# Kernel optimization log

Hardware: AMD Instinct MI355X
Metric: run time of the kernel (lower is better)

Reference implementation:

```python
import jax, jax.numpy as jnp
import numpy as np

NEG_SLOPE = 0.2  # PyG GATConv default leaky_relu slope


def gat_conv(h_in, src, dst, W, a_src, a_dst, b, N):
    # h_in: [N, Fin]; src/dst: [E] (self-loops already appended)
    h = h_in @ W                      # [N, Fout]
    alpha_src = h @ a_src             # [N]
    alpha_dst = h @ a_dst             # [N]
    e = jax.nn.leaky_relu(alpha_src[src] + alpha_dst[dst], NEG_SLOPE)  # [E]
    # segment softmax over incoming edges of each destination node
    m = jax.ops.segment_max(e, dst, num_segments=N)
    m = jnp.where(jnp.isfinite(m), m, 0.0)
    p = jnp.exp(e - m[dst])
    denom = jax.ops.segment_sum(p, dst, num_segments=N)
    alpha = p / jnp.maximum(denom[dst], 1e-16)
    out = jax.ops.segment_sum(alpha[:, None] * h[src], dst, num_segments=N)
    return out + b


def setup_inputs() -> dict:
    key = jax.random.key(0)
    ks = jax.random.split(key, 16)
    N, E, V, D, H, C, G = 100000, 1600000, 128, 50, 16, 10, 512
    x = jax.random.normal(ks[0], (N, V), dtype=jnp.float32)
    edge_index = jax.random.randint(ks[1], (2, E), 0, N, dtype=jnp.int32)
    batch = jnp.sort(jax.random.randint(ks[2], (N,), 0, G, dtype=jnp.int32))
    s = lambda fan: 1.0 / np.sqrt(fan)
    return {
        "x": x, "edge_index": edge_index, "batch": batch,
        "embedding": jax.random.normal(ks[3], (V, D), dtype=jnp.float32),
        "W1": jax.random.normal(ks[4], (D, H), dtype=jnp.float32) * s(D),
        "a_src1": jax.random.normal(ks[5], (H,), dtype=jnp.float32) * s(H),
        "a_dst1": jax.random.normal(ks[6], (H,), dtype=jnp.float32) * s(H),
        "b1": jnp.zeros((H,), dtype=jnp.float32),
        "W2": jax.random.normal(ks[7], (H, H), dtype=jnp.float32) * s(H),
        "a_src2": jax.random.normal(ks[8], (H,), dtype=jnp.float32) * s(H),
        "a_dst2": jax.random.normal(ks[9], (H,), dtype=jnp.float32) * s(H),
        "b2": jnp.zeros((H,), dtype=jnp.float32),
        "W3": jax.random.normal(ks[10], (H, C), dtype=jnp.float32) * s(H),
        "a_src3": jax.random.normal(ks[11], (C,), dtype=jnp.float32) * s(C),
        "a_dst3": jax.random.normal(ks[12], (C,), dtype=jnp.float32) * s(C),
        "b3": jnp.zeros((C,), dtype=jnp.float32),
    }


def reference(x, edge_index, batch, embedding, W1, a_src1, a_dst1, b1,
              W2, a_src2, a_dst2, b2, W3, a_src3, a_dst3, b3):
    N = x.shape[0]
    G = 512  # num graphs
    # embedding lookup via argmax over one-hot-ish features
    idx = jnp.argmax(x, axis=1)
    h = embedding[idx]                               # [N, 50]
    # add self-loops once (PyG GATConv default)
    loops = jnp.arange(N, dtype=edge_index.dtype)
    src = jnp.concatenate([edge_index[0], loops])
    dst = jnp.concatenate([edge_index[1], loops])
    h = jax.nn.relu(gat_conv(h, src, dst, W1, a_src1, a_dst1, b1, N))
    # dropout: eval mode -> identity
    h = jax.nn.relu(gat_conv(h, src, dst, W2, a_src2, a_dst2, b2, N))
    h = gat_conv(h, src, dst, W3, a_src3, a_dst3, b3, N)  # [N, C]
    # global mean pool over graphs
    sums = jax.ops.segment_sum(h, batch, num_segments=G)
    cnts = jax.ops.segment_sum(jnp.ones((N,), h.dtype), batch, num_segments=G)
    pooled = sums / jnp.maximum(cnts, 1.0)[:, None]
    return jax.nn.softmax(pooled, axis=1)
```

## Files before the change

kernel.cpp:

```cpp
#include <hip/hip_runtime.h>
#include <math.h>

#define NEG_SLOPE 0.2f
#define NBUK_MAX 512

typedef float v4f __attribute__((ext_vector_type(4)));
typedef _Float16 h4v __attribute__((ext_vector_type(4)));

#define RECB 64

template <int B2>
__global__ void __launch_bounds__(1024)
k_histarg(const float* __restrict__ x, const int* __restrict__ edst, int E,
          int* __restrict__ histT, int NBUK, int* __restrict__ idx, int N, int V) {
    __shared__ int sh[NBUK_MAX];
    int t = threadIdx.x;
    if ((int)blockIdx.x < B2) {
        int b = blockIdx.x;
        for (int k = t; k < NBUK; k += 1024) sh[k] = 0;
        __syncthreads();
        long long ebeg = (long long)b * E / B2, eend = (long long)(b + 1) * E / B2;
        for (long long i = ebeg + t; i < eend; i += 1024)
            atomicAdd(&sh[edst[i] >> 8], 1);
        __syncthreads();
        for (int k = t; k < NBUK; k += 1024) histT[(long long)k * B2 + b] = sh[k];
    } else {
        int node = ((int)blockIdx.x - B2) * 32 + (t >> 5);
        int lane = t & 31;
        if (node >= N) return;
        const v4f* row = (const v4f*)(x + (long long)node * V);
        float bv = -INFINITY;
        int bi = 0x7fffffff;
        int nq = V >> 2;
        for (int q = lane; q < nq; q += 32) {
            v4f v = row[q];
            int base = q << 2;
            if (v.x > bv || (v.x == bv && base     < bi)) { bv = v.x; bi = base;     }
            if (v.y > bv || (v.y == bv && base + 1 < bi)) { bv = v.y; bi = base + 1; }
            if (v.z > bv || (v.z == bv && base + 2 < bi)) { bv = v.z; bi = base + 2; }
            if (v.w > bv || (v.w == bv && base + 3 < bi)) { bv = v.w; bi = base + 3; }
        }
        for (int off = 16; off > 0; off >>= 1) {
            float ov = __shfl_down(bv, off, 32);
            int   oi = __shfl_down(bi, off, 32);
            if (ov > bv || (ov == bv && oi < bi)) { bv = ov; bi = oi; }
        }
        if (lane == 0) idx[node] = bi;
    }
}

template <int FIN, int FOUT>
__global__ void __launch_bounds__(256)
k_scan_tr(const int* __restrict__ vals, int* __restrict__ excl, int* __restrict__ bsums, int M,
          const float* __restrict__ emb, const int* __restrict__ idx,
          const float* __restrict__ W, const float* __restrict__ a_src,
          const float* __restrict__ a_dst, char* __restrict__ rec,
          int N, int NB_SCAN) {
    __shared__ int s[256];
    __shared__ float sW[FIN * FOUT];
    __shared__ float sa[FOUT], sd[FOUT];
    int t = threadIdx.x;
    if ((int)blockIdx.x < NB_SCAN) {
        int i = blockIdx.x * 256 + t;
        int v = (i < M) ? vals[i] : 0;
        s[t] = v;
        __syncthreads();
        for (int off = 1; off < 256; off <<= 1) {
            int a = (t >= off) ? s[t - off] : 0;
            __syncthreads();
            s[t] += a;
            __syncthreads();
        }
        if (i < M) excl[i] = s[t] - v;
        if (t == 255) bsums[blockIdx.x] = s[255];
    } else {
        for (int i = t; i < FIN * FOUT; i += 256) sW[i] = W[i];
        if (t < FOUT) { sa[t] = a_src[t]; sd[t] = a_dst[t]; }
        __syncthreads();
        int n = ((int)blockIdx.x - NB_SCAN) * 256 + t;
        if (n >= N) return;
        float acc[FOUT];
#pragma unroll
        for (int f = 0; f < FOUT; f++) acc[f] = 0.f;
        const float* hr = emb + (long long)idx[n] * FIN;
        for (int k = 0; k < FIN; k++) {
            float v = hr[k];
#pragma unroll
            for (int f = 0; f < FOUT; f++) acc[f] += v * sW[k * FOUT + f];
        }
        float s1 = 0.f, s2 = 0.f;
        _Float16 hh[16];
#pragma unroll
        for (int f = 0; f < 16; f++) hh[f] = (_Float16)0.f;
#pragma unroll
        for (int f = 0; f < FOUT; f++) {
            hh[f] = (_Float16)acc[f];
            s1 += acc[f] * sa[f];
            s2 += acc[f] * sd[f];
        }
        char* r = rec + (long long)n * RECB;
        *(uint4*)(r)      = ((uint4*)hh)[0];
        *(uint4*)(r + 16) = ((uint4*)hh)[1];
        float2 am; am.x = s1; am.y = s2;
        *(float2*)(r + 32) = am;
    }
}

template <int B2>
__global__ void __launch_bounds__(1024)
k_scatB(const int* __restrict__ esrc, const int* __restrict__ edst, int E,
        const int* __restrict__ sexcl, const int* __restrict__ bsums,
        int* __restrict__ tmp, int NBUK) {
    __shared__ int cur[NBUK_MAX];
    __shared__ int bex[512];
    int t = threadIdx.x, b = blockIdx.x;
    if (t < 512) bex[t] = (t < NBUK) ? bsums[t] : 0;
    __syncthreads();
    for (int off = 1; off < 512; off <<= 1) {
        int a = (t < 512 && t >= off) ? bex[t - off] : 0;
        __syncthreads();
        if (t < 512) bex[t] += a;
        __syncthreads();
    }
    for (int k = t; k < NBUK; k += 1024)
        cur[k] = sexcl[(long long)k * B2 + b] + (k ? bex[k - 1] : 0);
    __syncthreads();
    long long ebeg = (long long)b * E / B2, eend = (long long)(b + 1) * E / B2;
    for (long long i = ebeg + t; i < eend; i += 1024) {
        int d = edst[i];
        int pos = atomicAdd(&cur[d >> 8], 1);
        tmp[pos] = ((d & 255) << 17) | esrc[i];
    }
}

template <int B2>
__global__ void __launch_bounds__(256)
k_binB(const int* __restrict__ sexcl, const int* __restrict__ bsums,
       const int* __restrict__ tmp, int* __restrict__ perm, char* __restrict__ recA,
       int* __restrict__ csr_src, int N, int NBUK, int E) {
    __shared__ int bx[512];
    __shared__ int cnt[256];
    __shared__ int h1[256];
    __shared__ int h2[256];
    __shared__ int sdv[256];
    __shared__ int ssc[256];
    __shared__ int cur[256];
    int t = threadIdx.x, b = blockIdx.x;
    bx[t]       = (t < NBUK)       ? bsums[t]       : 0;
    bx[t + 256] = (t + 256 < NBUK) ? bsums[t + 256] : 0;
    __syncthreads();
    for (int off = 1; off < 512; off <<= 1) {
        int a0 = (t >= off) ? bx[t - off] : 0;
        int a1 = (t + 256 >= off) ? bx[t + 256 - off] : 0;
        __syncthreads();
        bx[t] += a0;
        bx[t + 256] += a1;
        __syncthreads();
    }
    int t0 = sexcl[(long long)b * B2] + (b ? bx[b - 1] : 0);
    int t1 = (b + 1 < NBUK) ? (sexcl[(long long)(b + 1) * B2] + bx[b]) : E;
    cnt[t] = 0;
    __syncthreads();
    for (int i = t0 + t; i < t1; i += 256) atomicAdd(&cnt[tmp[i] >> 17], 1);
    __syncthreads();
    int d = b * 256 + t;
    bool valid = d < N;
    int dg = cnt[t];

    h1[t] = 0;
    __syncthreads();
    int key = 255 - min(dg, 255);
    if (valid) atomicAdd(&h1[key], 1);
    __syncthreads();
    int v = h1[t];
    h2[t] = v;
    __syncthreads();
    for (int off = 1; off < 256; off <<= 1) {
        int a = (t >= off) ? h2[t - off] : 0;
        __syncthreads();
        h2[t] += a;
        __syncthreads();
    }
    h1[t] = h2[t] - v;
    __syncthreads();
    int r = 0;
    if (valid) r = atomicAdd(&h1[key], 1);

    sdv[t] = 0;
    __syncthreads();
    if (valid) sdv[r] = dg;
    __syncthreads();
    int sv = sdv[t];
    ssc[t] = sv;
    __syncthreads();
    for (int off = 1; off < 256; off <<= 1) {
        int a = (t >= off) ? ssc[t - off] : 0;
        __syncthreads();
        ssc[t] += a;
        __syncthreads();
    }
    if (valid) {
        int base = t0 + ssc[r] - dg;
        cur[t] = base;
        perm[b * 256 + r] = d;
        int2 m; m.x = base; m.y = base + dg;
        *(int2*)(recA + (long long)d * RECB + 40) = m;
    }
    __syncthreads();
    for (int i = t0 + t; i < t1; i += 256) {
        int p = tmp[i];
        int pos = atomicAdd(&cur[p >> 17], 1);
        csr_src[pos] = p & 0x1FFFF;
    }
}

template <typename EPI>
__device__ __forceinline__ void gat_core4(const char* __restrict__ rec,
                                          const int* __restrict__ csr_src,
                                          int d, int l4, EPI epilogue) {
    const char* rd = rec + (long long)d * RECB;
    int4 meta = *(const int4*)(rd + 32);
    float as_d = __int_as_float(meta.x);
    float ad   = __int_as_float(meta.y);
    int r0 = meta.z, r1 = meta.w;

    float e0 = as_d + ad;
    e0 = (e0 >= 0.f) ? e0 : NEG_SLOPE * e0;
    float p0 = __expf(e0);
    h4v hd = *(const h4v*)(rd + l4 * 8);
    float a0 = p0 * (float)hd[0], a1 = p0 * (float)hd[1];
    float a2 = p0 * (float)hd[2], a3 = p0 * (float)hd[3];
    float psum = (l4 == 0) ? p0 : 0.f;

    int rem = r1 - r0;
    if (rem > 0) {
        int j = r0;
        int s = (l4 < rem) ? csr_src[j + l4] : d;
        float av = *(const float*)(rec + (long long)s * RECB + 32);
        while (true) {
            int remn = rem - 4;
            int s2 = d; float av2 = 0.f;
            if (remn > 0) {
                s2 = (l4 < remn) ? csr_src[j + 4 + l4] : d;
                av2 = *(const float*)(rec + (long long)s2 * RECB + 32);
            }
            float e = av + ad;
            e = (e >= 0.f) ? e : NEG_SLOPE * e;
            float p = (l4 < rem) ? __expf(e) : 0.f;
            psum += p;
#pragma unroll
            for (int k = 0; k < 4; k++) {
                float pk = __shfl(p, k, 4);
                int   sk = __shfl(s, k, 4);
                h4v hh = *(const h4v*)(rec + (long long)sk * RECB + l4 * 8);
                a0 += pk * (float)hh[0];
                a1 += pk * (float)hh[1];
                a2 += pk * (float)hh[2];
                a3 += pk * (float)hh[3];
            }
            if (remn <= 0) break;
            j += 4; rem = remn; s = s2; av = av2;
        }
    }
    psum += __shfl_xor(psum, 1, 4);
    psum += __shfl_xor(psum, 2, 4);
    float inv = 1.f / fmaxf(psum, 1e-16f);
    epilogue(d, r0, r1, a0 * inv, a1 * inv, a2 * inv, a3 * inv);
}

template <int FN>
__global__ void __launch_bounds__(256)
k_gat_ft(const char* __restrict__ rec, const int* __restrict__ csr_src,
         const int* __restrict__ perm, const float* __restrict__ bias,
         const float* __restrict__ Wn, const float* __restrict__ an_src,
         const float* __restrict__ an_dst, char* __restrict__ rec_next, int N) {
    __shared__ float sW[16 * 16];
    __shared__ float sa[16], sd[16], sb[16];
    int t = threadIdx.x;
    {
        int k = t >> 4, f = t & 15;
        sW[t] = (f < FN) ? Wn[k * FN + f] : 0.f;
    }
    if (t < 16) {
        sa[t] = (t < FN) ? an_src[t] : 0.f;
        sd[t] = (t < FN) ? an_dst[t] : 0.f;
        sb[t] = bias[t];
    }
    __syncthreads();

    int gid = blockIdx.x * 256 + t;
    int grp = gid >> 2, l4 = gid & 3;
    if (grp >= N) return;
    int d = perm[grp];

    gat_core4(rec, csr_src, d, l4,
        [&](int dd, int r0, int r1, float v0, float v1, float v2, float v3) {
            int f0 = l4 * 4;
            float vv[4];
            vv[0] = fmaxf(v0 + sb[f0    ], 0.f);
            vv[1] = fmaxf(v1 + sb[f0 + 1], 0.f);
            vv[2] = fmaxf(v2 + sb[f0 + 2], 0.f);
            vv[3] = fmaxf(v3 + sb[f0 + 3], 0.f);
            float o0 = 0.f, o1 = 0.f, o2 = 0.f, o3 = 0.f;
#pragma unroll
            for (int q = 0; q < 4; q++) {
#pragma unroll
                for (int i = 0; i < 4; i++) {
                    float vk = __shfl(vv[i], q, 4);
                    const float* wr = &sW[(q * 4 + i) * 16 + f0];
                    o0 += vk * wr[0];
                    o1 += vk * wr[1];
                    o2 += vk * wr[2];
                    o3 += vk * wr[3];
                }
            }
            float c1 = o0 * sa[f0] + o1 * sa[f0 + 1] + o2 * sa[f0 + 2] + o3 * sa[f0 + 3];
            float c2 = o0 * sd[f0] + o1 * sd[f0 + 1] + o2 * sd[f0 + 2] + o3 * sd[f0 + 3];
            c1 += __shfl_xor(c1, 1, 4); c1 += __shfl_xor(c1, 2, 4);
            c2 += __shfl_xor(c2, 1, 4); c2 += __shfl_xor(c2, 2, 4);
            char* rn = rec_next + (long long)dd * RECB;
            h4v ho = { (_Float16)o0, (_Float16)o1, (_Float16)o2, (_Float16)o3 };
            *(h4v*)(rn + l4 * 8) = ho;
            if (l4 == 0) {
                int4 m;
                m.x = __float_as_int(c1); m.y = __float_as_int(c2);
                m.z = r0; m.w = r1;
                *(int4*)(rn + 32) = m;
            }
        });
}

__global__ void __launch_bounds__(256)
k_gat_last(const char* __restrict__ rec, const int* __restrict__ csr_src,
           const int* __restrict__ perm, float* __restrict__ out, int N) {
    int gid = blockIdx.x * 256 + threadIdx.x;
    int grp = gid >> 2, l4 = gid & 3;
    if (grp >= N) return;
    int d = perm[grp];
    gat_core4(rec, csr_src, d, l4,
        [&](int dd, int r0, int r1, float v0, float v1, float v2, float v3) {
            v4f o = { v0, v1, v2, v3 };
            ((v4f*)out)[(long long)dd * 4 + l4] = o;
        });
}

__global__ void k_pool(const float* __restrict__ h3, const int* __restrict__ batch,
                       const float* __restrict__ b3, float* __restrict__ out, int N, int C) {
    int g = blockIdx.x;
    int lo = 0, hi = N;
    while (lo < hi) { int mid = (lo + hi) >> 1; if (batch[mid] < g) lo = mid + 1; else hi = mid; }
    int start = lo;
    hi = N;
    while (lo < hi) { int mid = (lo + hi) >> 1; if (batch[mid] < g + 1) lo = mid + 1; else hi = mid; }
    int end = lo;

    float sum[16];
    for (int f = 0; f < C; f++) sum[f] = 0.f;
    for (int n = start + threadIdx.x; n < end; n += blockDim.x) {
        const float* r = h3 + (long long)n * 16;
        for (int f = 0; f < C; f++) sum[f] += r[f];
    }
    __shared__ float red[256 * 16];
    for (int f = 0; f < C; f++) red[threadIdx.x * 16 + f] = sum[f];
    __syncthreads();
    for (int str = blockDim.x / 2; str > 0; str >>= 1) {
        if ((int)threadIdx.x < str)
            for (int f = 0; f < C; f++) red[threadIdx.x * 16 + f] += red[(threadIdx.x + str) * 16 + f];
        __syncthreads();
    }
    if (threadIdx.x == 0) {
        float cnt = fmaxf((float)(end - start), 1.f);
        float vals[16];
        float mx = -INFINITY;
        for (int f = 0; f < C; f++) { vals[f] = red[f] / cnt + b3[f]; mx = fmaxf(mx, vals[f]); }
        float se = 0.f;
        for (int f = 0; f < C; f++) { vals[f] = __expf(vals[f] - mx); se += vals[f]; }
        for (int f = 0; f < C; f++) out[(long long)g * C + f] = vals[f] / se;
    }
}

extern "C" void kernel_launch(void* const* d_in, const int* in_sizes, int n_in,
                              void* d_out, int out_size, void* d_ws, size_t ws_size,
                              hipStream_t stream) {
    const float* x    = (const float*)d_in[0];
    const int*   eidx = (const int*)d_in[1];
    const int*   batch= (const int*)d_in[2];
    const float* emb  = (const float*)d_in[3];
    const float* W1   = (const float*)d_in[4];
    const float* as1  = (const float*)d_in[5];
    const float* ad1  = (const float*)d_in[6];
    const float* b1   = (const float*)d_in[7];
    const float* W2   = (const float*)d_in[8];
    const float* as2  = (const float*)d_in[9];
    const float* ad2  = (const float*)d_in[10];
    const float* b2   = (const float*)d_in[11];
    const float* W3   = (const float*)d_in[12];
    const float* as3  = (const float*)d_in[13];
    const float* ad3  = (const float*)d_in[14];
    const float* b3   = (const float*)d_in[15];

    const int H = in_sizes[5];
    const int C = in_sizes[13];
    const int D = in_sizes[4] / H;
    const int V = in_sizes[3] / D;
    const int N = in_sizes[0] / V;
    const int E = in_sizes[1] / 2;
    const int G = out_size / C;
    const int* esrc = eidx;
    const int* edst = eidx + E;
    const int NBUK = (N + 255) >> 8;
    constexpr int B2 = 256;
    const int M = NBUK * B2;

    char* w = (char*)d_ws;
    auto carve = [&](size_t bytes) {
        char* p = w;
        w += (bytes + 255) & ~(size_t)255;
        return p;
    };
    int*   idx     = (int*)carve((size_t)N * 4);
    int*   perm    = (int*)carve((size_t)N * 4);
    int*   histT   = (int*)carve((size_t)M * 4);
    int*   sexcl   = (int*)carve((size_t)M * 4);
    int*   bsums   = (int*)carve(2048 * 4);
    int*   csr_src = (int*)carve((size_t)E * 4);
    char*  recA    = carve((size_t)N * RECB);
    char*  recB    = carve((size_t)N * RECB);
    size_t zone_bytes = ((size_t)E * 4 > (size_t)N * 64) ? (size_t)E * 4 : (size_t)N * 64;
    char*  zone = carve(zone_bytes);
    float* X0  = (float*)zone;
    int*   tmp = (int*)zone;
    (void)ws_size; (void)n_in;

    const int BT = 256;
    dim3 blk(BT);
    int gGat4 = (N * 4 + BT - 1) / BT;
    int nb2   = (M + 255) / 256;
    int gArg  = (N + 31) / 32;
    int gTr   = (N + BT - 1) / BT;

    k_histarg<B2><<<B2 + gArg, dim3(1024), 0, stream>>>(x, edst, E, histT, NBUK, idx, N, V);

    k_scan_tr<50, 16><<<nb2 + gTr, blk, 0, stream>>>(histT, sexcl, bsums, M,
                                                     emb, idx, W1, as1, ad1, recA, N, nb2);

    k_scatB<B2><<<B2, dim3(1024), 0, stream>>>(esrc, edst, E, sexcl, bsums, tmp, NBUK);
    k_binB<B2><<<NBUK, blk, 0, stream>>>(sexcl, bsums, tmp, perm, recA, csr_src, N, NBUK, E);

    k_gat_ft<16><<<gGat4, blk, 0, stream>>>(recA, csr_src, perm, b1, W2, as2, ad2, recB, N);

    k_gat_ft<10><<<gGat4, blk, 0, stream>>>(recB, csr_src, perm, b2, W3, as3, ad3, recA, N);

    k_gat_last<<<gGat4, blk, 0, stream>>>(recA, csr_src, perm, X0, N);

    k_pool<<<G, blk, 0, stream>>>(X0, batch, b3, (float*)d_out, N, C);
}
```

Before: 303.3 us.

## Split node records into separate feature, alpha-src and meta arrays; add nontemporal hints

Replaces the 64-byte per-node record with three arrays: fp16 features (32B/node), a compact float array of source attention scores, and a 16-byte meta array. The gather of alpha_src for neighbors now touches a dense 4-byte array instead of strided 64-byte records, improving cache hit rate for random edge gathers. Also adds nontemporal loads/stores on streaming edge data, x, csr_src and outputs to reduce cache pollution. Risk: nontemporal hints on csr_src reads in the GAT loop may hurt if they were reused across layers.

```diff
diff --git a/kernel.cpp b/kernel.cpp
--- a/kernel.cpp
+++ b/kernel.cpp
@@ -7,7 +7,6 @@
 typedef float v4f __attribute__((ext_vector_type(4)));
 typedef _Float16 h4v __attribute__((ext_vector_type(4)));
 
-#define RECB 64
 
 template <int B2>
 __global__ void __launch_bounds__(1024)
@@ -21,7 +20,7 @@
         __syncthreads();
         long long ebeg = (long long)b * E / B2, eend = (long long)(b + 1) * E / B2;
         for (long long i = ebeg + t; i < eend; i += 1024)
-            atomicAdd(&sh[edst[i] >> 8], 1);
+            atomicAdd(&sh[__builtin_nontemporal_load(&edst[i]) >> 8], 1);
         __syncthreads();
         for (int k = t; k < NBUK; k += 1024) histT[(long long)k * B2 + b] = sh[k];
     } else {
@@ -33,7 +32,7 @@
         int bi = 0x7fffffff;
         int nq = V >> 2;
         for (int q = lane; q < nq; q += 32) {
-            v4f v = row[q];
+            v4f v = __builtin_nontemporal_load(&row[q]);
             int base = q << 2;
             if (v.x > bv || (v.x == bv && base     < bi)) { bv = v.x; bi = base;     }
             if (v.y > bv || (v.y == bv && base + 1 < bi)) { bv = v.y; bi = base + 1; }
@@ -54,7 +53,8 @@
 k_scan_tr(const int* __restrict__ vals, int* __restrict__ excl, int* __restrict__ bsums, int M,
           const float* __restrict__ emb, const int* __restrict__ idx,
           const float* __restrict__ W, const float* __restrict__ a_src,
-          const float* __restrict__ a_dst, char* __restrict__ rec,
+          const float* __restrict__ a_dst, _Float16* __restrict__ hT,
+          float* __restrict__ asrc, int4* __restrict__ meta,
           int N, int NB_SCAN) {
     __shared__ int s[256];
     __shared__ float sW[FIN * FOUT];
@@ -98,11 +98,12 @@
             s1 += acc[f] * sa[f];
             s2 += acc[f] * sd[f];
         }
-        char* r = rec + (long long)n * RECB;
-        *(uint4*)(r)      = ((uint4*)hh)[0];
-        *(uint4*)(r + 16) = ((uint4*)hh)[1];
+        uint4* hrow = (uint4*)(hT + (long long)n * 16);
+        hrow[0] = ((uint4*)hh)[0];
+        hrow[1] = ((uint4*)hh)[1];
+        asrc[n] = s1;
         float2 am; am.x = s1; am.y = s2;
-        *(float2*)(r + 32) = am;
+        *(float2*)&meta[n] = am;
     }
 }
 
@@ -127,16 +128,17 @@
     __syncthreads();
     long long ebeg = (long long)b * E / B2, eend = (long long)(b + 1) * E / B2;
     for (long long i = ebeg + t; i < eend; i += 1024) {
-        int d = edst[i];
+        int d = __builtin_nontemporal_load(&edst[i]);
+        int sv = __builtin_nontemporal_load(&esrc[i]);
         int pos = atomicAdd(&cur[d >> 8], 1);
-        tmp[pos] = ((d & 255) << 17) | esrc[i];
+        __builtin_nontemporal_store(((d & 255) << 17) | sv, &tmp[pos]);
     }
 }
 
 template <int B2>
 __global__ void __launch_bounds__(256)
 k_binB(const int* __restrict__ sexcl, const int* __restrict__ bsums,
-       const int* __restrict__ tmp, int* __restrict__ perm, char* __restrict__ recA,
+       const int* __restrict__ tmp, int* __restrict__ perm, int4* __restrict__ meta,
        int* __restrict__ csr_src, int N, int NBUK, int E) {
     __shared__ int bx[512];
     __shared__ int cnt[256];
@@ -161,7 +163,8 @@
     int t1 = (b + 1 < NBUK) ? (sexcl[(long long)(b + 1) * B2] + bx[b]) : E;
     cnt[t] = 0;
     __syncthreads();
-    for (int i = t0 + t; i < t1; i += 256) atomicAdd(&cnt[tmp[i] >> 17], 1);
+    for (int i = t0 + t; i < t1; i += 256)
+        atomicAdd(&cnt[__builtin_nontemporal_load(&tmp[i]) >> 17], 1);
     __syncthreads();
     int d = b * 256 + t;
     bool valid = d < N;
@@ -204,30 +207,32 @@
         cur[t] = base;
         perm[b * 256 + r] = d;
         int2 m; m.x = base; m.y = base + dg;
-        *(int2*)(recA + (long long)d * RECB + 40) = m;
+        *(int2*)((char*)&meta[d] + 8) = m;
     }
     __syncthreads();
     for (int i = t0 + t; i < t1; i += 256) {
-        int p = tmp[i];
+        int p = __builtin_nontemporal_load(&tmp[i]);
         int pos = atomicAdd(&cur[p >> 17], 1);
-        csr_src[pos] = p & 0x1FFFF;
+        __builtin_nontemporal_store(p & 0x1FFFF, &csr_src[pos]);
     }
 }
 
 template <typename EPI>
-__device__ __forceinline__ void gat_core4(const char* __restrict__ rec,
+__device__ __forceinline__ void gat_core4(const _Float16* __restrict__ hT,
+                                          const float* __restrict__ asrc,
+                                          const int4* __restrict__ meta,
                                           const int* __restrict__ csr_src,
                                           int d, int l4, EPI epilogue) {
-    const char* rd = rec + (long long)d * RECB;
-    int4 meta = *(const int4*)(rd + 32);
-    float as_d = __int_as_float(meta.x);
-    float ad   = __int_as_float(meta.y);
-    int r0 = meta.z, r1 = meta.w;
+    const h4v* __restrict__ H = (const h4v*)hT;
+    int4 m = meta[d];
+    float as_d = __int_as_float(m.x);
+    float ad   = __int_as_float(m.y);
+    int r0 = m.z, r1 = m.w;
 
     float e0 = as_d + ad;
     e0 = (e0 >= 0.f) ? e0 : NEG_SLOPE * e0;
     float p0 = __expf(e0);
-    h4v hd = *(const h4v*)(rd + l4 * 8);
+    h4v hd = H[(long long)d * 4 + l4];
     float a0 = p0 * (float)hd[0], a1 = p0 * (float)hd[1];
     float a2 = p0 * (float)hd[2], a3 = p0 * (float)hd[3];
     float psum = (l4 == 0) ? p0 : 0.f;
@@ -235,14 +240,14 @@
     int rem = r1 - r0;
     if (rem > 0) {
         int j = r0;
-        int s = (l4 < rem) ? csr_src[j + l4] : d;
-        float av = *(const float*)(rec + (long long)s * RECB + 32);
+        int s = (l4 < rem) ? __builtin_nontemporal_load(&csr_src[j + l4]) : d;
+        float av = asrc[s];
         while (true) {
             int remn = rem - 4;
             int s2 = d; float av2 = 0.f;
             if (remn > 0) {
-                s2 = (l4 < remn) ? csr_src[j + 4 + l4] : d;
-                av2 = *(const float*)(rec + (long long)s2 * RECB + 32);
+                s2 = (l4 < remn) ? __builtin_nontemporal_load(&csr_src[j + 4 + l4]) : d;
+                av2 = asrc[s2];
             }
             float e = av + ad;
             e = (e >= 0.f) ? e : NEG_SLOPE * e;
@@ -252,7 +257,7 @@
             for (int k = 0; k < 4; k++) {
                 float pk = __shfl(p, k, 4);
                 int   sk = __shfl(s, k, 4);
-                h4v hh = *(const h4v*)(rec + (long long)sk * RECB + l4 * 8);
+                h4v hh = H[(long long)sk * 4 + l4];
                 a0 += pk * (float)hh[0];
                 a1 += pk * (float)hh[1];
                 a2 += pk * (float)hh[2];
@@ -270,10 +275,13 @@
 
 template <int FN>
 __global__ void __launch_bounds__(256)
-k_gat_ft(const char* __restrict__ rec, const int* __restrict__ csr_src,
+k_gat_ft(const _Float16* __restrict__ hT, const float* __restrict__ asrc,
+         const int4* __restrict__ meta, const int* __restrict__ csr_src,
          const int* __restrict__ perm, const float* __restrict__ bias,
          const float* __restrict__ Wn, const float* __restrict__ an_src,
-         const float* __restrict__ an_dst, char* __restrict__ rec_next, int N) {
+         const float* __restrict__ an_dst,
+         _Float16* __restrict__ hT_n, float* __restrict__ asrc_n,
+         int4* __restrict__ meta_n, int N) {
     __shared__ float sW[16 * 16];
     __shared__ float sa[16], sd[16], sb[16];
     int t = threadIdx.x;
@@ -293,7 +301,7 @@
     if (grp >= N) return;
     int d = perm[grp];
 
-    gat_core4(rec, csr_src, d, l4,
+    gat_core4(hT, asrc, meta, csr_src, d, l4,
         [&](int dd, int r0, int r1, float v0, float v1, float v2, float v3) {
             int f0 = l4 * 4;
             float vv[4];
@@ -318,29 +326,30 @@
             float c2 = o0 * sd[f0] + o1 * sd[f0 + 1] + o2 * sd[f0 + 2] + o3 * sd[f0 + 3];
             c1 += __shfl_xor(c1, 1, 4); c1 += __shfl_xor(c1, 2, 4);
             c2 += __shfl_xor(c2, 1, 4); c2 += __shfl_xor(c2, 2, 4);
-            char* rn = rec_next + (long long)dd * RECB;
             h4v ho = { (_Float16)o0, (_Float16)o1, (_Float16)o2, (_Float16)o3 };
-            *(h4v*)(rn + l4 * 8) = ho;
+            ((h4v*)hT_n)[(long long)dd * 4 + l4] = ho;
             if (l4 == 0) {
+                asrc_n[dd] = c1;
                 int4 m;
                 m.x = __float_as_int(c1); m.y = __float_as_int(c2);
                 m.z = r0; m.w = r1;
-                *(int4*)(rn + 32) = m;
+                meta_n[dd] = m;
             }
         });
 }
 
 __global__ void __launch_bounds__(256)
-k_gat_last(const char* __restrict__ rec, const int* __restrict__ csr_src,
+k_gat_last(const _Float16* __restrict__ hT, const float* __restrict__ asrc,
+           const int4* __restrict__ meta, const int* __restrict__ csr_src,
            const int* __restrict__ perm, float* __restrict__ out, int N) {
     int gid = blockIdx.x * 256 + threadIdx.x;
     int grp = gid >> 2, l4 = gid & 3;
     if (grp >= N) return;
     int d = perm[grp];
-    gat_core4(rec, csr_src, d, l4,
+    gat_core4(hT, asrc, meta, csr_src, d, l4,
         [&](int dd, int r0, int r1, float v0, float v1, float v2, float v3) {
             v4f o = { v0, v1, v2, v3 };
-            ((v4f*)out)[(long long)dd * 4 + l4] = o;
+            __builtin_nontemporal_store(o, &((v4f*)out)[(long long)dd * 4 + l4]);
         });
 }
 
@@ -358,7 +367,7 @@
     for (int f = 0; f < C; f++) sum[f] = 0.f;
     for (int n = start + threadIdx.x; n < end; n += blockDim.x) {
         const float* r = h3 + (long long)n * 16;
-        for (int f = 0; f < C; f++) sum[f] += r[f];
+        for (int f = 0; f < C; f++) sum[f] += __builtin_nontemporal_load(&r[f]);
     }
     __shared__ float red[256 * 16];
     for (int f = 0; f < C; f++) red[threadIdx.x * 16 + f] = sum[f];
@@ -418,14 +427,18 @@
         w += (bytes + 255) & ~(size_t)255;
         return p;
     };
-    int*   idx     = (int*)carve((size_t)N * 4);
-    int*   perm    = (int*)carve((size_t)N * 4);
-    int*   histT   = (int*)carve((size_t)M * 4);
-    int*   sexcl   = (int*)carve((size_t)M * 4);
-    int*   bsums   = (int*)carve(2048 * 4);
-    int*   csr_src = (int*)carve((size_t)E * 4);
-    char*  recA    = carve((size_t)N * RECB);
-    char*  recB    = carve((size_t)N * RECB);
+    int*      idx     = (int*)carve((size_t)N * 4);
+    int*      perm    = (int*)carve((size_t)N * 4);
+    int*      histT   = (int*)carve((size_t)M * 4);
+    int*      sexcl   = (int*)carve((size_t)M * 4);
+    int*      bsums   = (int*)carve(2048 * 4);
+    int*      csr_src = (int*)carve((size_t)E * 4);
+    _Float16* hTa     = (_Float16*)carve((size_t)N * 32);
+    _Float16* hTb     = (_Float16*)carve((size_t)N * 32);
+    float*    asA     = (float*)carve((size_t)N * 4);
+    float*    asB     = (float*)carve((size_t)N * 4);
+    int4*     metaA   = (int4*)carve((size_t)N * 16);
+    int4*     metaB   = (int4*)carve((size_t)N * 16);
     size_t zone_bytes = ((size_t)E * 4 > (size_t)N * 64) ? (size_t)E * 4 : (size_t)N * 64;
     char*  zone = carve(zone_bytes);
     float* X0  = (float*)zone;
@@ -442,16 +455,19 @@
     k_histarg<B2><<<B2 + gArg, dim3(1024), 0, stream>>>(x, edst, E, histT, NBUK, idx, N, V);
 
     k_scan_tr<50, 16><<<nb2 + gTr, blk, 0, stream>>>(histT, sexcl, bsums, M,
-                                                     emb, idx, W1, as1, ad1, recA, N, nb2);
+                                                     emb, idx, W1, as1, ad1,
+                                                     hTa, asA, metaA, N, nb2);
 
     k_scatB<B2><<<B2, dim3(1024), 0, stream>>>(esrc, edst, E, sexcl, bsums, tmp, NBUK);
-    k_binB<B2><<<NBUK, blk, 0, stream>>>(sexcl, bsums, tmp, perm, recA, csr_src, N, NBUK, E);
-
-    k_gat_ft<16><<<gGat4, blk, 0, stream>>>(recA, csr_src, perm, b1, W2, as2, ad2, recB, N);
-
-    k_gat_ft<10><<<gGat4, blk, 0, stream>>>(recB, csr_src, perm, b2, W3, as3, ad3, recA, N);
-
-    k_gat_last<<<gGat4, blk, 0, stream>>>(recA, csr_src, perm, X0, N);
+    k_binB<B2><<<NBUK, blk, 0, stream>>>(sexcl, bsums, tmp, perm, metaA, csr_src, N, NBUK, E);
+
+    k_gat_ft<16><<<gGat4, blk, 0, stream>>>(hTa, asA, metaA, csr_src, perm, b1,
+                                            W2, as2, ad2, hTb, asB, metaB, N);
+
+    k_gat_ft<10><<<gGat4, blk, 0, stream>>>(hTb, asB, metaB, csr_src, perm, b2,
+                                            W3, as3, ad3, hTa, asA, metaA, N);
+
+    k_gat_last<<<gGat4, blk, 0, stream>>>(hTa, asA, metaA, csr_src, perm, X0, N);
 
     k_pool<<<G, blk, 0, stream>>>(X0, batch, b3, (float*)d_out, N, C);
 }
```

New measurement: 369.8 us. 21.9% more time.
